# Kernel tuning notes

Hardware: AMD Instinct MI355X
Metric: run time of the kernel (lower is better)

Reference implementation:

```python
import jax, jax.numpy as jnp
import numpy as np

N_Q = 50000
B, T = 256, 500
DK = 128      # q_embed_dim == memory_key_state_dim == final_fc_dim
DV = 256      # qa_embed_dim == memory_value_state_dim
M = 50        # memory_size

def setup_inputs() -> dict:
    key = jax.random.key(0)
    ks = jax.random.split(key, 12)
    q_data = jax.random.randint(ks[0], (B, T), 0, N_Q + 1)
    qa_data = jax.random.randint(ks[1], (B, T), 0, 2 * N_Q + 1)
    # target in {-1, 0, 1}; -1 = padding (masked out)
    u = jax.random.uniform(ks[2], (B * T, 1))
    target = jnp.floor(u * 3.0) - 1.0
    # embedding tables with padding_idx=0 zeroed
    q_tab = (jax.random.normal(ks[3], (N_Q + 1, DK)) * (2.0 / DK) ** 0.5).at[0].set(0.0)
    qa_tab = (jax.random.normal(ks[4], (2 * N_Q + 1, DV)) * (2.0 / DV) ** 0.5).at[0].set(0.0)
    Mk = jax.random.normal(ks[5], (M, DK)) * (2.0 / DK) ** 0.5
    Mv0 = jax.random.normal(ks[6], (M, DV)) * (2.0 / DV) ** 0.5
    We = jax.random.normal(ks[7], (DV, DV)) * (1.0 / DV) ** 0.5
    be = jnp.zeros((DV,))
    Wa = jax.random.normal(ks[8], (DV, DV)) * (1.0 / DV) ** 0.5
    ba = jnp.zeros((DV,))
    Wr = jax.random.normal(ks[9], (DK, DV + DK)) * (2.0 / (DV + DK)) ** 0.5
    br = jnp.zeros((DK,))
    Wp = jax.random.normal(ks[10], (1, DK)) * (2.0 / DK) ** 0.5
    bp = jnp.zeros((1,))
    return dict(q_data=q_data, qa_data=qa_data, target=target, q_tab=q_tab,
                qa_tab=qa_tab, Mk=Mk, Mv0=Mv0, We=We, be=be, Wa=Wa, ba=ba,
                Wr=Wr, br=br, Wp=Wp, bp=bp)


def reference(q_data, qa_data, target, q_tab, qa_tab, Mk, Mv0, We, be, Wa, ba, Wr, br, Wp, bp):
    b, t = q_data.shape
    q_e = q_tab[q_data]            # (B,T,DK)
    qa_e = qa_tab[qa_data]         # (B,T,DV)
    wr_mask = (q_data >= 1).astype(q_e.dtype)  # write gate per step
    Mv_init = jnp.broadcast_to(Mv0[None], (b, M, DV))

    def step(Mv, xs):
        q, qa, m = xs              # q:(B,DK) qa:(B,DV) m:(B,)
        w = jax.nn.softmax(q @ Mk.T, axis=-1)          # (B,M) correlation weight
        read = jnp.einsum('bm,bmd->bd', w, Mv)         # (B,DV)
        e = jax.nn.sigmoid(qa @ We.T + be)             # erase (B,DV)
        a = jnp.tanh(qa @ Wa.T + ba)                   # add   (B,DV)
        new = Mv * (1.0 - w[:, :, None] * e[:, None, :]) + w[:, :, None] * a[:, None, :]
        Mv = jnp.where(m[:, None, None] > 0, new, Mv)  # only write for non-pad steps
        return Mv, read

    _, reads = jax.lax.scan(step, Mv_init,
                            (q_e.transpose(1, 0, 2), qa_e.transpose(1, 0, 2), wr_mask.T))
    reads = reads.transpose(1, 0, 2)                    # (B,T,DV)
    feat = jnp.concatenate([reads, q_e], axis=2).reshape(b * t, DV + DK)
    h = jnp.tanh(feat @ Wr.T + br)                      # (B*T,DK)
    pred = h @ Wp.T + bp                                # (B*T,1) logits
    mask = target >= 0
    # stable BCE-with-logits per element
    per = jnp.maximum(pred, 0.0) - pred * target + jnp.log1p(jnp.exp(-jnp.abs(pred)))
    n_valid = jnp.maximum(jnp.sum(mask.astype(pred.dtype)), 1.0)
    loss = jnp.sum(jnp.where(mask, per, 0.0)) / n_valid
    probs = jax.nn.sigmoid(pred)
    return loss, probs
```

## Files before the change

kernel.cpp:

```cpp
#include <hip/hip_runtime.h>
#include <hip/hip_bf16.h>
#include <stdint.h>


#define BATCH 256
#define TLEN  500
#define DKQ   128
#define DVV   256
#define MSZ   50
#define NROWS 128000
#define GSZ   10

__device__ __forceinline__ float bfs(uint16_t u){
  union { uint32_t u; float f; } v; v.u = ((uint32_t)u) << 16; return v.f;
}
__device__ __forceinline__ uint16_t f2b(float x){
  union { __hip_bfloat16 h; uint16_t u; } c; c.h = __float2bfloat16(x); return c.u;
}

typedef __attribute__((ext_vector_type(8))) short bf16x8;
typedef __attribute__((ext_vector_type(4))) float f32x4;

__global__ __launch_bounds__(128, 1) void k_w(
    const int* __restrict__ q_data, const float* __restrict__ q_tab,
    const float* __restrict__ Mk, float* __restrict__ w_ws)
{
  __shared__ float mk[MSZ*DKQ];
  __shared__ float wt[128*52];
  const int tid = threadIdx.x;
  for (int li = tid; li < 1600; li += 128)
    ((float4*)mk)[li] = ((const float4*)Mk)[li];
  __syncthreads();

  const int row = blockIdx.x*128 + tid;
  const int qi = q_data[row];
  const float4* qrow = (const float4*)(q_tab + (size_t)qi*DKQ);

  float acc[MSZ];
  #pragma unroll
  for (int m=0;m<MSZ;m++) acc[m] = 0.f;

  #pragma unroll 1
  for (int c8=0; c8<8; c8++){
    float4 q0 = qrow[c8*4+0], q1 = qrow[c8*4+1], q2 = qrow[c8*4+2], q3 = qrow[c8*4+3];
    #pragma unroll
    for (int m=0;m<MSZ;m++){
      const float4* mr = (const float4*)&mk[m*DKQ + c8*16];
      float4 a = mr[0], b = mr[1], cc = mr[2], d = mr[3];
      float s = acc[m];
      s = fmaf(q0.x,a.x,s);  s = fmaf(q0.y,a.y,s);  s = fmaf(q0.z,a.z,s);  s = fmaf(q0.w,a.w,s);
      s = fmaf(q1.x,b.x,s);  s = fmaf(q1.y,b.y,s);  s = fmaf(q1.z,b.z,s);  s = fmaf(q1.w,b.w,s);
      s = fmaf(q2.x,cc.x,s); s = fmaf(q2.y,cc.y,s); s = fmaf(q2.z,cc.z,s); s = fmaf(q2.w,cc.w,s);
      s = fmaf(q3.x,d.x,s);  s = fmaf(q3.y,d.y,s);  s = fmaf(q3.z,d.z,s);  s = fmaf(q3.w,d.w,s);
      acc[m] = s;
    }
  }
  float mx = acc[0];
  #pragma unroll
  for (int m=1;m<MSZ;m++) mx = fmaxf(mx, acc[m]);
  float s = 0.f;
  #pragma unroll
  for (int m=0;m<MSZ;m++){ acc[m] = __expf(acc[m]-mx); s += acc[m]; }
  float inv = 1.0f / s;
  #pragma unroll
  for (int m=0;m<MSZ;m++) wt[tid*52+m] = acc[m]*inv;
  wt[tid*52+50] = 0.f; wt[tid*52+51] = 0.f;
  __syncthreads();
  float4* dst = (float4*)(w_ws + (size_t)blockIdx.x*128*52);
  const float4* src = (const float4*)wt;
  for (int li = tid; li < 1664; li += 128) dst[li] = src[li];
}

__global__ __launch_bounds__(256) void k_cvt(
    const float* __restrict__ qa_tab, uint16_t* __restrict__ qa_bf)
{
  const size_t n4 = 6400064;
  size_t stride = (size_t)gridDim.x*blockDim.x;
  for (size_t i = (size_t)blockIdx.x*256 + threadIdx.x; i < n4; i += stride){
    float4 v = ((const float4*)qa_tab)[i];
    ushort4 o;
    o.x = f2b(v.x); o.y = f2b(v.y); o.z = f2b(v.z); o.w = f2b(v.w);
    ((ushort4*)qa_bf)[i] = o;
  }
}

__device__ __forceinline__ void gl_lds16(const void* g, void* l){
  __builtin_amdgcn_global_load_lds(
      (const __attribute__((address_space(1))) void*)g,
      (__attribute__((address_space(3))) void*)l, 16, 0, 0);
}

__global__ __launch_bounds__(256, 2) void k_ea(
    const int* __restrict__ qa_data, const uint16_t* __restrict__ qa_bf,
    const float* __restrict__ We, const float* __restrict__ Wa,
    const float* __restrict__ be, const float* __restrict__ ba,
    __hip_bfloat16* __restrict__ ea_ws)
{
  __shared__ uint16_t Ab[128*32];
  __shared__ uint16_t Bb[128*32];
  const int tid = threadIdx.x;
  const int lane = tid & 63, wid = tid >> 6;
  const int nb = blockIdx.x & 3, mb = blockIdx.x >> 2;
  const int rb = mb*128, cb = nb*128;

  const char* qac = (const char*)qa_bf;
  size_t aoff0, aoff1;
  {
    int r0 = wid*32 + (lane>>2);
    aoff0 = (size_t)qa_data[rb + r0]*512      + (size_t)(lane&3)*16;
    aoff1 = (size_t)qa_data[rb + r0 + 16]*512 + (size_t)(lane&3)*16;
  }
  const float* Wsrc = (nb < 2) ? We : Wa;
  const int cb2 = (nb & 1)*128;

  const int wr = (wid>>1)*64, wc = (wid&1)*64;
  float bias[4];
  #pragma unroll
  for (int tj=0;tj<4;tj++){
    int colg = cb + wc + tj*16 + (lane&15);
    bias[tj] = (nb<2) ? be[colg] : ba[colg-256];
  }

  f32x4 acc[4][4];
  #pragma unroll
  for (int i=0;i<4;i++){
    #pragma unroll
    for (int j=0;j<4;j++) acc[i][j] = (f32x4)(0.f);
  }

  #pragma unroll 1
  for (int kc=0; kc<8; kc++){
    __syncthreads();
    gl_lds16(qac + aoff0 + (size_t)kc*64, &Ab[(wid*2+0)*512]);
    gl_lds16(qac + aoff1 + (size_t)kc*64, &Ab[(wid*2+1)*512]);
    #pragma unroll
    for (int it=0; it<4; it++){
      int li = tid*4 + it;
      int col = li >> 3, kq = li & 7;
      float4 v = ((const float4*)(Wsrc + (size_t)(cb2+col)*256 + kc*32))[kq];
      ushort4 o;
      o.x = f2b(v.x); o.y = f2b(v.y); o.z = f2b(v.z); o.w = f2b(v.w);
      *(ushort4*)&Bb[col*32 + kq*4] = o;
    }
    __syncthreads();
    bf16x8 af[4], bfr[4];
    #pragma unroll
    for (int ti=0;ti<4;ti++)
      af[ti] = *(const bf16x8*)&Ab[(wr + ti*16 + (lane&15))*32 + (lane>>4)*8];
    #pragma unroll
    for (int tj=0;tj<4;tj++)
      bfr[tj] = *(const bf16x8*)&Bb[(wc + tj*16 + (lane&15))*32 + (lane>>4)*8];
    #pragma unroll
    for (int ti=0;ti<4;ti++){
      #pragma unroll
      for (int tj=0;tj<4;tj++)
        acc[ti][tj] = __builtin_amdgcn_mfma_f32_16x16x32_bf16(af[ti], bfr[tj], acc[ti][tj], 0, 0, 0);
    }
  }
  const int rq = (lane>>4)*4, cl = lane&15;
  #pragma unroll
  for (int ti=0;ti<4;ti++){
    #pragma unroll
    for (int r=0;r<4;r++){
      int row = rb + wr + ti*16 + rq + r;
      __hip_bfloat16* orow = ea_ws + (size_t)row*512 + cb + wc;
      #pragma unroll
      for (int tj=0;tj<4;tj++){
        float x = acc[ti][tj][r] + bias[tj];
        float v = (nb<2) ? (1.f/(1.f+__expf(-x)))
                         : (1.f - 2.f/(__expf(2.f*x)+1.f));
        orow[tj*16 + cl] = __float2bfloat16(v);
      }
    }
  }
}

__global__ __launch_bounds__(256, 1) void k_scan(
    const int* __restrict__ q_data, const float* __restrict__ w_ws,
    const uint16_t* __restrict__ ea_ws, const float* __restrict__ Mv0,
    __hip_bfloat16* __restrict__ reads_ws)
{
  __shared__ float wbuf[2][GSZ*52];
  const int b = blockIdx.x, d = threadIdx.x;
  float Mv[MSZ];
  #pragma unroll
  for (int m=0;m<MSZ;m++) Mv[m] = Mv0[m*256 + d];
  const int base = b*TLEN;

  float4 wreg;
  uint16_t ecur[GSZ], acur[GSZ], enxt[GSZ], anxt[GSZ];
  int qcur[GSZ], qnxt[GSZ];

  if (d < 130) wreg = ((const float4*)(w_ws + (size_t)base*52))[d];
  #pragma unroll
  for (int j=0;j<GSZ;j++){
    ecur[j] = ea_ws[(size_t)(base+j)*512 + d];
    acur[j] = ea_ws[(size_t)(base+j)*512 + 256 + d];
    qcur[j] = q_data[base+j];
  }
  if (d < 130) ((float4*)wbuf[0])[d] = wreg;
  __syncthreads();

  #pragma unroll 1
  for (int g=0; g<50; g++){
    if (g < 49){
      const int sn = base + (g+1)*GSZ;
      if (d < 130) wreg = ((const float4*)(w_ws + (size_t)sn*52))[d];
      #pragma unroll
      for (int j=0;j<GSZ;j++){
        enxt[j] = ea_ws[(size_t)(sn+j)*512 + d];
        anxt[j] = ea_ws[(size_t)(sn+j)*512 + 256 + d];
        qnxt[j] = q_data[sn+j];
      }
    }
    const float* wb = wbuf[g&1];
    const int s0 = base + g*GSZ;
    #pragma unroll
    for (int j=0;j<GSZ;j++){
      float4 wv[13];
      #pragma unroll
      for (int q=0;q<13;q++) wv[q] = ((const float4*)(wb + j*52))[q];
      float ef = bfs(ecur[j]), af = bfs(acur[j]);
      float r0=0.f, r1=0.f, r2=0.f, r3=0.f;
      #pragma unroll
      for (int q=0;q<13;q++){
        const int mb = q*4;
        r0 = fmaf(wv[q].x, Mv[mb], r0);
        if (mb+1<MSZ) r1 = fmaf(wv[q].y, Mv[mb+1], r1);
        if (mb+2<MSZ) r2 = fmaf(wv[q].z, Mv[mb+2], r2);
        if (mb+3<MSZ) r3 = fmaf(wv[q].w, Mv[mb+3], r3);
      }
      float rd = (r0+r1)+(r2+r3);
      reads_ws[(size_t)(s0+j)*256 + d] = __float2bfloat16(rd);
      if (qcur[j] > 0){
        #pragma unroll
        for (int q=0;q<13;q++){
          const int mb = q*4;
          { float tt = fmaf(ef, Mv[mb], -af);   Mv[mb]   = fmaf(-wv[q].x, tt, Mv[mb]); }
          if (mb+1<MSZ){ float tt = fmaf(ef, Mv[mb+1], -af); Mv[mb+1] = fmaf(-wv[q].y, tt, Mv[mb+1]); }
          if (mb+2<MSZ){ float tt = fmaf(ef, Mv[mb+2], -af); Mv[mb+2] = fmaf(-wv[q].z, tt, Mv[mb+2]); }
          if (mb+3<MSZ){ float tt = fmaf(ef, Mv[mb+3], -af); Mv[mb+3] = fmaf(-wv[q].w, tt, Mv[mb+3]); }
        }
      }
    }
    if (g < 49){
      if (d < 130) ((float4*)wbuf[(g+1)&1])[d] = wreg;
      #pragma unroll
      for (int j=0;j<GSZ;j++){ ecur[j]=enxt[j]; acur[j]=anxt[j]; qcur[j]=qnxt[j]; }
    }
    __syncthreads();
  }
}

__global__ __launch_bounds__(256, 2) void k_final(
    const int* __restrict__ q_data, const float* __restrict__ q_tab,
    const uint16_t* __restrict__ reads16, const float* __restrict__ Wr,
    const float* __restrict__ br, const float* __restrict__ Wp,
    const float* __restrict__ bp, const float* __restrict__ target,
    float* __restrict__ out, float* __restrict__ parts)
{
  __shared__ uint16_t Ab[64*32];
  __shared__ uint16_t Bb[128*32];
  __shared__ float redbuf[8];
  const int tid = threadIdx.x;
  const int lane = tid & 63, wid = tid >> 6;
  const int rb = blockIdx.x * 64;

  f32x4 acc[8];
  #pragma unroll
  for (int tj=0;tj<8;tj++) acc[tj] = (f32x4)(0.f);

  #pragma unroll 1
  for (int kc=0; kc<12; kc++){
    __syncthreads();
    if (kc < 8){
      int row = tid >> 2, seg = tid & 3;
      *(uint4*)&Ab[row*32 + seg*8] =
        *(const uint4*)&reads16[(size_t)(rb+row)*256 + kc*32 + seg*8];
    } else {
      #pragma unroll
      for (int it=0; it<2; it++){
        int li = it*256 + tid;
        int row = li >> 3, seg = li & 7;
        float4 v = *(const float4*)&q_tab[(size_t)q_data[rb+row]*DKQ + (kc-8)*32 + seg*4];
        ushort4 o; o.x=f2b(v.x); o.y=f2b(v.y); o.z=f2b(v.z); o.w=f2b(v.w);
        *(ushort4*)&Ab[row*32 + seg*4] = o;
      }
    }
    #pragma unroll
    for (int it=0; it<4; it++){
      int li = it*256 + tid;
      int col = li >> 3, seg = li & 7;
      float4 v = *(const float4*)&Wr[(size_t)col*384 + kc*32 + seg*4];
      ushort4 o; o.x=f2b(v.x); o.y=f2b(v.y); o.z=f2b(v.z); o.w=f2b(v.w);
      *(ushort4*)&Bb[col*32 + seg*4] = o;
    }
    __syncthreads();
    bf16x8 af = *(const bf16x8*)&Ab[(wid*16 + (lane&15))*32 + (lane>>4)*8];
    #pragma unroll
    for (int tj=0;tj<8;tj++){
      bf16x8 bf = *(const bf16x8*)&Bb[(tj*16 + (lane&15))*32 + (lane>>4)*8];
      acc[tj] = __builtin_amdgcn_mfma_f32_16x16x32_bf16(af, bf, acc[tj], 0, 0, 0);
    }
  }
  const int cl = lane & 15, rq = lane >> 4;
  float p[4] = {0.f,0.f,0.f,0.f};
  #pragma unroll
  for (int tj=0;tj<8;tj++){
    int cg = tj*16 + cl;
    float brv = br[cg], wpv = Wp[cg];
    #pragma unroll
    for (int r=0;r<4;r++){
      float x = acc[tj][r] + brv;
      float h = 1.f - 2.f/(__expf(2.f*x)+1.f);
      p[r] = fmaf(h, wpv, p[r]);
    }
  }
  #pragma unroll
  for (int off=1; off<16; off<<=1){
    #pragma unroll
    for (int r=0;r<4;r++) p[r] += __shfl_xor(p[r], off);
  }
  float bpv = bp[0];
  float lsum = 0.f, csum = 0.f;
  if (cl == 0){
    #pragma unroll
    for (int r=0;r<4;r++){
      int row = rb + wid*16 + rq*4 + r;
      float pred = p[r] + bpv;
      out[1 + row] = 1.f/(1.f + __expf(-pred));
      float tg = target[row];
      if (tg >= 0.f){
        lsum += fmaxf(pred, 0.f) - pred*tg + log1pf(__expf(-fabsf(pred)));
        csum += 1.f;
      }
    }
  }
  #pragma unroll
  for (int off=16; off<64; off<<=1){
    lsum += __shfl_xor(lsum, off);
    csum += __shfl_xor(csum, off);
  }
  if (lane == 0){ redbuf[wid*2] = lsum; redbuf[wid*2+1] = csum; }
  __syncthreads();
  if (tid == 0){
    parts[blockIdx.x]        = redbuf[0]+redbuf[2]+redbuf[4]+redbuf[6];
    parts[2000 + blockIdx.x] = redbuf[1]+redbuf[3]+redbuf[5]+redbuf[7];
  }
}

__global__ __launch_bounds__(256) void k_loss(
    const float* __restrict__ parts, float* __restrict__ out)
{
  __shared__ float red[8];
  const int tid = threadIdx.x;
  float l = 0.f, cn = 0.f;
  for (int i = tid; i < 2000; i += 256){ l += parts[i]; cn += parts[2000+i]; }
  #pragma unroll
  for (int off=32; off>0; off>>=1){ l += __shfl_xor(l, off); cn += __shfl_xor(cn, off); }
  if ((tid & 63) == 0){ red[(tid>>6)*2] = l; red[(tid>>6)*2+1] = cn; }
  __syncthreads();
  if (tid == 0){
    float L = red[0]+red[2]+red[4]+red[6];
    float C = red[1]+red[3]+red[5]+red[7];
    out[0] = L / fmaxf(C, 1.f);
  }
}

extern "C" void kernel_launch(void* const* d_in, const int* in_sizes, int n_in,
                              void* d_out, int out_size, void* d_ws, size_t ws_size,
                              hipStream_t stream) {
  const int*   q_data  = (const int*)d_in[0];
  const int*   qa_data = (const int*)d_in[1];
  const float* target  = (const float*)d_in[2];
  const float* q_tab   = (const float*)d_in[3];
  const float* qa_tab  = (const float*)d_in[4];
  const float* Mk  = (const float*)d_in[5];
  const float* Mv0 = (const float*)d_in[6];
  const float* We  = (const float*)d_in[7];
  const float* be  = (const float*)d_in[8];
  const float* Wa  = (const float*)d_in[9];
  const float* ba  = (const float*)d_in[10];
  const float* Wr  = (const float*)d_in[11];
  const float* br  = (const float*)d_in[12];
  const float* Wp  = (const float*)d_in[13];
  const float* bp  = (const float*)d_in[14];

  char* ws = (char*)d_ws;
  float*          w_ws     = (float*)ws;
  __hip_bfloat16* ea_ws    = (__hip_bfloat16*)(ws + 26624000);
  uint16_t*       qa_bf    = (uint16_t*)(ws + 157696000);
  __hip_bfloat16* reads_ws = (__hip_bfloat16*)(ws + 157696000);
  float*          parts    = (float*)ws;

  float* out = (float*)d_out;

  k_w    <<<1000, 128, 0, stream>>>(q_data, q_tab, Mk, w_ws);
  k_cvt  <<<2048, 256, 0, stream>>>(qa_tab, qa_bf);
  k_ea   <<<4000, 256, 0, stream>>>(qa_data, qa_bf, We, Wa, be, ba, ea_ws);
  k_scan <<<256,  256, 0, stream>>>(q_data, w_ws, (const uint16_t*)ea_ws, Mv0, reads_ws);
  k_final<<<2000, 256, 0, stream>>>(q_data, q_tab, (const uint16_t*)reads_ws, Wr, br, Wp, bp, target, out, parts);
  k_loss <<<1,    256, 0, stream>>>(parts, out);
}
```

Measured before the change: 674.6 us.

## Preconvert weights to bf16, use LDS-direct loads, split scan memory across two halves

We/Wa and Wr plus the q table are converted to bf16 once in conversion kernels. The GEMM kernels then stage tiles with global_load_lds instead of per-block fp32 loads and conversions. k_ea block indices are remapped so the four column blocks of a row tile launch close together, improving reuse of the gathered rows. The scan kernel doubles its thread count, with each half owning about half of the 50 memory slots, and combines partial reads through shared memory. That halves per-thread register work but adds a __syncthreads per time step. An extra q_tab conversion pass over about 25MB is also added.

```diff
diff --git a/kernel.cpp b/kernel.cpp
--- a/kernel.cpp
+++ b/kernel.cpp
@@ -20,6 +20,12 @@
 
 typedef __attribute__((ext_vector_type(8))) short bf16x8;
 typedef __attribute__((ext_vector_type(4))) float f32x4;
+
+__device__ __forceinline__ void gl_lds16(const void* g, void* l){
+  __builtin_amdgcn_global_load_lds(
+      (const __attribute__((address_space(1))) void*)g,
+      (__attribute__((address_space(3))) void*)l, 16, 0, 0);
+}
 
 __global__ __launch_bounds__(128, 1) void k_w(
     const int* __restrict__ q_data, const float* __restrict__ q_tab,
@@ -72,35 +78,65 @@
 }
 
 __global__ __launch_bounds__(256) void k_cvt(
-    const float* __restrict__ qa_tab, uint16_t* __restrict__ qa_bf)
-{
-  const size_t n4 = 6400064;
+    const float* __restrict__ qa_tab, const float* __restrict__ We,
+    const float* __restrict__ Wa, uint16_t* __restrict__ qa_bf,
+    uint16_t* __restrict__ wcomb)
+{
+  const size_t n_qa4 = 6400064;
+  const size_t n_w4  = 32768;
   size_t stride = (size_t)gridDim.x*blockDim.x;
-  for (size_t i = (size_t)blockIdx.x*256 + threadIdx.x; i < n4; i += stride){
-    float4 v = ((const float4*)qa_tab)[i];
-    ushort4 o;
-    o.x = f2b(v.x); o.y = f2b(v.y); o.z = f2b(v.z); o.w = f2b(v.w);
-    ((ushort4*)qa_bf)[i] = o;
-  }
-}
-
-__device__ __forceinline__ void gl_lds16(const void* g, void* l){
-  __builtin_amdgcn_global_load_lds(
-      (const __attribute__((address_space(1))) void*)g,
-      (__attribute__((address_space(3))) void*)l, 16, 0, 0);
+  for (size_t i = (size_t)blockIdx.x*256 + threadIdx.x; i < n_qa4 + n_w4; i += stride){
+    float4 v;
+    if (i < n_qa4){
+      v = ((const float4*)qa_tab)[i];
+      ushort4 o; o.x=f2b(v.x); o.y=f2b(v.y); o.z=f2b(v.z); o.w=f2b(v.w);
+      ((ushort4*)qa_bf)[i] = o;
+    } else {
+      size_t j = i - n_qa4;
+      size_t f = j*4;
+      int col = (int)(f >> 8), k = (int)(f & 255);
+      const float* srcp = (col < 256) ? (We + (size_t)col*256 + k)
+                                      : (Wa + (size_t)(col-256)*256 + k);
+      v = *(const float4*)srcp;
+      ushort4 o; o.x=f2b(v.x); o.y=f2b(v.y); o.z=f2b(v.z); o.w=f2b(v.w);
+      ((ushort4*)wcomb)[j] = o;
+    }
+  }
+}
+
+__global__ __launch_bounds__(256) void k_cvt2(
+    const float* __restrict__ q_tab, const float* __restrict__ Wr,
+    uint16_t* __restrict__ q_bf, uint16_t* __restrict__ wr_bf)
+{
+  const size_t n_q4  = 1600032;
+  const size_t n_wr4 = 12288;
+  size_t stride = (size_t)gridDim.x*blockDim.x;
+  for (size_t i = (size_t)blockIdx.x*256 + threadIdx.x; i < n_q4 + n_wr4; i += stride){
+    if (i < n_q4){
+      float4 v = ((const float4*)q_tab)[i];
+      ushort4 o; o.x=f2b(v.x); o.y=f2b(v.y); o.z=f2b(v.z); o.w=f2b(v.w);
+      ((ushort4*)q_bf)[i] = o;
+    } else {
+      size_t j = i - n_q4;
+      float4 v = ((const float4*)Wr)[j];
+      ushort4 o; o.x=f2b(v.x); o.y=f2b(v.y); o.z=f2b(v.z); o.w=f2b(v.w);
+      ((ushort4*)wr_bf)[j] = o;
+    }
+  }
 }
 
 __global__ __launch_bounds__(256, 2) void k_ea(
     const int* __restrict__ qa_data, const uint16_t* __restrict__ qa_bf,
-    const float* __restrict__ We, const float* __restrict__ Wa,
-    const float* __restrict__ be, const float* __restrict__ ba,
-    __hip_bfloat16* __restrict__ ea_ws)
+    const uint16_t* __restrict__ wcomb, const float* __restrict__ be,
+    const float* __restrict__ ba, __hip_bfloat16* __restrict__ ea_ws)
 {
   __shared__ uint16_t Ab[128*32];
   __shared__ uint16_t Bb[128*32];
   const int tid = threadIdx.x;
   const int lane = tid & 63, wid = tid >> 6;
-  const int nb = blockIdx.x & 3, mb = blockIdx.x >> 2;
+  const int braw = blockIdx.x;
+  const int nb = (braw >> 3) & 3;
+  const int mb = (braw & 7) | ((braw >> 5) << 3);
   const int rb = mb*128, cb = nb*128;
 
   const char* qac = (const char*)qa_bf;
@@ -110,8 +146,9 @@
     aoff0 = (size_t)qa_data[rb + r0]*512      + (size_t)(lane&3)*16;
     aoff1 = (size_t)qa_data[rb + r0 + 16]*512 + (size_t)(lane&3)*16;
   }
-  const float* Wsrc = (nb < 2) ? We : Wa;
-  const int cb2 = (nb & 1)*128;
+  const char* wcb = (const char*)wcomb;
+  size_t boff0 = (size_t)(cb + wid*32 + (lane>>2))*512 + (size_t)(lane&3)*16;
+  size_t boff1 = boff0 + 16*512;
 
   const int wr = (wid>>1)*64, wc = (wid&1)*64;
   float bias[4];
@@ -133,15 +170,8 @@
     __syncthreads();
     gl_lds16(qac + aoff0 + (size_t)kc*64, &Ab[(wid*2+0)*512]);
     gl_lds16(qac + aoff1 + (size_t)kc*64, &Ab[(wid*2+1)*512]);
-    #pragma unroll
-    for (int it=0; it<4; it++){
-      int li = tid*4 + it;
-      int col = li >> 3, kq = li & 7;
-      float4 v = ((const float4*)(Wsrc + (size_t)(cb2+col)*256 + kc*32))[kq];
-      ushort4 o;
-      o.x = f2b(v.x); o.y = f2b(v.y); o.z = f2b(v.z); o.w = f2b(v.w);
-      *(ushort4*)&Bb[col*32 + kq*4] = o;
-    }
+    gl_lds16(wcb + boff0 + (size_t)kc*64, &Bb[(wid*2+0)*512]);
+    gl_lds16(wcb + boff1 + (size_t)kc*64, &Bb[(wid*2+1)*512]);
     __syncthreads();
     bf16x8 af[4], bfr[4];
     #pragma unroll
@@ -175,37 +205,46 @@
   }
 }
 
-__global__ __launch_bounds__(256, 1) void k_scan(
+__global__ __launch_bounds__(512, 1) void k_scan(
     const int* __restrict__ q_data, const float* __restrict__ w_ws,
     const uint16_t* __restrict__ ea_ws, const float* __restrict__ Mv0,
     __hip_bfloat16* __restrict__ reads_ws)
 {
   __shared__ float wbuf[2][GSZ*52];
-  const int b = blockIdx.x, d = threadIdx.x;
-  float Mv[MSZ];
-  #pragma unroll
-  for (int m=0;m<MSZ;m++) Mv[m] = Mv0[m*256 + d];
-  const int base = b*TLEN;
+  __shared__ float part[2][256];
+  const int tid = threadIdx.x;
+  const int d = tid & 255, h = tid >> 8;
+  const int base = blockIdx.x*TLEN;
+
+  float Mv[28];
+  #pragma unroll
+  for (int qq=0; qq<7; qq++){
+    #pragma unroll
+    for (int e=0;e<4;e++){
+      int quad = 2*qq + h, m = quad*4 + e;
+      Mv[qq*4+e] = (quad <= 12 && m < MSZ) ? Mv0[m*256 + d] : 0.f;
+    }
+  }
 
   float4 wreg;
   uint16_t ecur[GSZ], acur[GSZ], enxt[GSZ], anxt[GSZ];
   int qcur[GSZ], qnxt[GSZ];
 
-  if (d < 130) wreg = ((const float4*)(w_ws + (size_t)base*52))[d];
+  if (tid < 130) wreg = ((const float4*)(w_ws + (size_t)base*52))[tid];
   #pragma unroll
   for (int j=0;j<GSZ;j++){
     ecur[j] = ea_ws[(size_t)(base+j)*512 + d];
     acur[j] = ea_ws[(size_t)(base+j)*512 + 256 + d];
     qcur[j] = q_data[base+j];
   }
-  if (d < 130) ((float4*)wbuf[0])[d] = wreg;
+  if (tid < 130) ((float4*)wbuf[0])[tid] = wreg;
   __syncthreads();
 
   #pragma unroll 1
   for (int g=0; g<50; g++){
     if (g < 49){
       const int sn = base + (g+1)*GSZ;
-      if (d < 130) wreg = ((const float4*)(w_ws + (size_t)sn*52))[d];
+      if (tid < 130) wreg = ((const float4*)(w_ws + (size_t)sn*52))[tid];
       #pragma unroll
       for (int j=0;j<GSZ;j++){
         enxt[j] = ea_ws[(size_t)(sn+j)*512 + d];
@@ -217,34 +256,49 @@
     const int s0 = base + g*GSZ;
     #pragma unroll
     for (int j=0;j<GSZ;j++){
-      float4 wv[13];
-      #pragma unroll
-      for (int q=0;q<13;q++) wv[q] = ((const float4*)(wb + j*52))[q];
+      const float4* wq = (const float4*)(wb + j*52);
       float ef = bfs(ecur[j]), af = bfs(acur[j]);
+      float4 wv[7];
+      #pragma unroll
+      for (int qq=0; qq<6; qq++) wv[qq] = wq[2*qq + h];
+      if (h == 0) wv[6] = wq[12];
       float r0=0.f, r1=0.f, r2=0.f, r3=0.f;
       #pragma unroll
-      for (int q=0;q<13;q++){
-        const int mb = q*4;
-        r0 = fmaf(wv[q].x, Mv[mb], r0);
-        if (mb+1<MSZ) r1 = fmaf(wv[q].y, Mv[mb+1], r1);
-        if (mb+2<MSZ) r2 = fmaf(wv[q].z, Mv[mb+2], r2);
-        if (mb+3<MSZ) r3 = fmaf(wv[q].w, Mv[mb+3], r3);
-      }
-      float rd = (r0+r1)+(r2+r3);
-      reads_ws[(size_t)(s0+j)*256 + d] = __float2bfloat16(rd);
+      for (int qq=0; qq<6; qq++){
+        r0 = fmaf(wv[qq].x, Mv[qq*4+0], r0);
+        r1 = fmaf(wv[qq].y, Mv[qq*4+1], r1);
+        r2 = fmaf(wv[qq].z, Mv[qq*4+2], r2);
+        r3 = fmaf(wv[qq].w, Mv[qq*4+3], r3);
+      }
+      if (h == 0){
+        r0 = fmaf(wv[6].x, Mv[24], r0);
+        r1 = fmaf(wv[6].y, Mv[25], r1);
+        r2 = fmaf(wv[6].z, Mv[26], r2);
+        r3 = fmaf(wv[6].w, Mv[27], r3);
+      }
+      float rp = (r0+r1)+(r2+r3);
+      if (h == 0) part[j&1][d] = rp;
+      __syncthreads();
+      if (h == 1){
+        float rd = rp + part[j&1][d];
+        reads_ws[(size_t)(s0+j)*256 + d] = __float2bfloat16(rd);
+      }
       if (qcur[j] > 0){
         #pragma unroll
-        for (int q=0;q<13;q++){
-          const int mb = q*4;
-          { float tt = fmaf(ef, Mv[mb], -af);   Mv[mb]   = fmaf(-wv[q].x, tt, Mv[mb]); }
-          if (mb+1<MSZ){ float tt = fmaf(ef, Mv[mb+1], -af); Mv[mb+1] = fmaf(-wv[q].y, tt, Mv[mb+1]); }
-          if (mb+2<MSZ){ float tt = fmaf(ef, Mv[mb+2], -af); Mv[mb+2] = fmaf(-wv[q].z, tt, Mv[mb+2]); }
-          if (mb+3<MSZ){ float tt = fmaf(ef, Mv[mb+3], -af); Mv[mb+3] = fmaf(-wv[q].w, tt, Mv[mb+3]); }
+        for (int qq=0; qq<6; qq++){
+          { float tt = fmaf(ef, Mv[qq*4+0], -af); Mv[qq*4+0] = fmaf(-wv[qq].x, tt, Mv[qq*4+0]); }
+          { float tt = fmaf(ef, Mv[qq*4+1], -af); Mv[qq*4+1] = fmaf(-wv[qq].y, tt, Mv[qq*4+1]); }
+          { float tt = fmaf(ef, Mv[qq*4+2], -af); Mv[qq*4+2] = fmaf(-wv[qq].z, tt, Mv[qq*4+2]); }
+          { float tt = fmaf(ef, Mv[qq*4+3], -af); Mv[qq*4+3] = fmaf(-wv[qq].w, tt, Mv[qq*4+3]); }
         }
+        if (h == 0){
+          { float tt = fmaf(ef, Mv[24], -af); Mv[24] = fmaf(-wv[6].x, tt, Mv[24]); }
+          { float tt = fmaf(ef, Mv[25], -af); Mv[25] = fmaf(-wv[6].y, tt, Mv[25]); }
+        }
       }
     }
     if (g < 49){
-      if (d < 130) ((float4*)wbuf[(g+1)&1])[d] = wreg;
+      if (tid < 130) ((float4*)wbuf[(g+1)&1])[tid] = wreg;
       #pragma unroll
       for (int j=0;j<GSZ;j++){ ecur[j]=enxt[j]; acur[j]=anxt[j]; qcur[j]=qnxt[j]; }
     }
@@ -253,8 +307,8 @@
 }
 
 __global__ __launch_bounds__(256, 2) void k_final(
-    const int* __restrict__ q_data, const float* __restrict__ q_tab,
-    const uint16_t* __restrict__ reads16, const float* __restrict__ Wr,
+    const int* __restrict__ q_data, const uint16_t* __restrict__ q_bf,
+    const uint16_t* __restrict__ reads16, const uint16_t* __restrict__ wr_bf,
     const float* __restrict__ br, const float* __restrict__ Wp,
     const float* __restrict__ bp, const float* __restrict__ target,
     float* __restrict__ out, float* __restrict__ parts)
@@ -266,6 +320,15 @@
   const int lane = tid & 63, wid = tid >> 6;
   const int rb = blockIdx.x * 64;
 
+  const char* rdc = (const char*)reads16;
+  const char* qbc = (const char*)q_bf;
+  const char* wrc = (const char*)wr_bf;
+  const int arow = wid*16 + (lane>>2);
+  size_t aoff_r = (size_t)(rb+arow)*512 + (size_t)(lane&3)*16;
+  size_t aoff_q = (size_t)q_data[rb+arow]*256 + (size_t)(lane&3)*16;
+  size_t boff0  = (size_t)(wid*32 + (lane>>2))*768 + (size_t)(lane&3)*16;
+  size_t boff1  = boff0 + 16*768;
+
   f32x4 acc[8];
   #pragma unroll
   for (int tj=0;tj<8;tj++) acc[tj] = (f32x4)(0.f);
@@ -273,28 +336,10 @@
   #pragma unroll 1
   for (int kc=0; kc<12; kc++){
     __syncthreads();
-    if (kc < 8){
-      int row = tid >> 2, seg = tid & 3;
-      *(uint4*)&Ab[row*32 + seg*8] =
-        *(const uint4*)&reads16[(size_t)(rb+row)*256 + kc*32 + seg*8];
-    } else {
-      #pragma unroll
-      for (int it=0; it<2; it++){
-        int li = it*256 + tid;
-        int row = li >> 3, seg = li & 7;
-        float4 v = *(const float4*)&q_tab[(size_t)q_data[rb+row]*DKQ + (kc-8)*32 + seg*4];
-        ushort4 o; o.x=f2b(v.x); o.y=f2b(v.y); o.z=f2b(v.z); o.w=f2b(v.w);
-        *(ushort4*)&Ab[row*32 + seg*4] = o;
-      }
-    }
-    #pragma unroll
-    for (int it=0; it<4; it++){
-      int li = it*256 + tid;
-      int col = li >> 3, seg = li & 7;
-      float4 v = *(const float4*)&Wr[(size_t)col*384 + kc*32 + seg*4];
-      ushort4 o; o.x=f2b(v.x); o.y=f2b(v.y); o.z=f2b(v.z); o.w=f2b(v.w);
-      *(ushort4*)&Bb[col*32 + seg*4] = o;
-    }
+    if (kc < 8) gl_lds16(rdc + aoff_r + (size_t)kc*64,     &Ab[wid*512]);
+    else        gl_lds16(qbc + aoff_q + (size_t)(kc-8)*64, &Ab[wid*512]);
+    gl_lds16(wrc + boff0 + (size_t)kc*64, &Bb[(wid*2+0)*512]);
+    gl_lds16(wrc + boff1 + (size_t)kc*64, &Bb[(wid*2+1)*512]);
     __syncthreads();
     bf16x8 af = *(const bf16x8*)&Ab[(wid*16 + (lane&15))*32 + (lane>>4)*8];
     #pragma unroll
@@ -312,8 +357,8 @@
     #pragma unroll
     for (int r=0;r<4;r++){
       float x = acc[tj][r] + brv;
-      float h = 1.f - 2.f/(__expf(2.f*x)+1.f);
-      p[r] = fmaf(h, wpv, p[r]);
+      float hh = 1.f - 2.f/(__expf(2.f*x)+1.f);
+      p[r] = fmaf(hh, wpv, p[r]);
     }
   }
   #pragma unroll
@@ -390,15 +435,19 @@
   float*          w_ws     = (float*)ws;
   __hip_bfloat16* ea_ws    = (__hip_bfloat16*)(ws + 26624000);
   uint16_t*       qa_bf    = (uint16_t*)(ws + 157696000);
+  uint16_t*       wcomb    = (uint16_t*)(ws + 208896512);
   __hip_bfloat16* reads_ws = (__hip_bfloat16*)(ws + 157696000);
   float*          parts    = (float*)ws;
+  uint16_t*       q_bf     = (uint16_t*)(ws + 2000000);
+  uint16_t*       wr_bf    = (uint16_t*)(ws + 16000000);
 
   float* out = (float*)d_out;
 
   k_w    <<<1000, 128, 0, stream>>>(q_data, q_tab, Mk, w_ws);
-  k_cvt  <<<2048, 256, 0, stream>>>(qa_tab, qa_bf);
-  k_ea   <<<4000, 256, 0, stream>>>(qa_data, qa_bf, We, Wa, be, ba, ea_ws);
-  k_scan <<<256,  256, 0, stream>>>(q_data, w_ws, (const uint16_t*)ea_ws, Mv0, reads_ws);
-  k_final<<<2000, 256, 0, stream>>>(q_data, q_tab, (const uint16_t*)reads_ws, Wr, br, Wp, bp, target, out, parts);
+  k_cvt  <<<2048, 256, 0, stream>>>(qa_tab, We, Wa, qa_bf, wcomb);
+  k_ea   <<<4000, 256, 0, stream>>>(qa_data, qa_bf, wcomb, be, ba, ea_ws);
+  k_scan <<<256,  512, 0, stream>>>(q_data, w_ws, (const uint16_t*)ea_ws, Mv0, reads_ws);
+  k_cvt2 <<<1024, 256, 0, stream>>>(q_tab, Wr, q_bf, wr_bf);
+  k_final<<<2000, 256, 0, stream>>>(q_data, q_bf, (const uint16_t*)reads_ws, wr_bf, br, Wp, bp, target, out, parts);
   k_loss <<<1,    256, 0, stream>>>(parts, out);
 }
```

Measured after the change: 653.0 us. -3.2%, faster.
